# Kernel optimization log

Measured on AMD Instinct MI355X. Metric: run time of the kernel, lower is better.

## Reference

```python
import jax, jax.numpy as jnp
import numpy as np

RES = (160, 160, 160)
SCENE_MIN = -1.0
SCENE_SIZE = 2.0
NEAR, FAR = 0.1, 10.0
NUM_SAMPLES = 128


def eval_sh_deg2(dirs):
    # dirs: [N, 3] -> SH basis [N, 9] (degree 2)
    d = dirs / (jnp.linalg.norm(dirs, axis=-1, keepdims=True) + 1e-8)
    x, y, z = d[..., 0], d[..., 1], d[..., 2]
    return jnp.stack([
        0.28209479177387814 * jnp.ones_like(x),
        -0.48860251190291987 * y,
        0.48860251190291987 * z,
        -0.48860251190291987 * x,
        1.0925484305920792 * x * y,
        -1.0925484305920792 * y * z,
        0.31539156525252005 * (2.0 * z * z - x * x - y * y),
        -1.0925484305920792 * x * z,
        0.5462742152960396 * (x * x - y * y),
    ], axis=-1)


def trilinear_interp(coords, density, sh_coeffs):
    # coords: [N, 3] world coords; grids indexed [z, y, x] as in the torch source
    res = jnp.asarray(RES, dtype=coords.dtype)
    vox = (coords - SCENE_MIN) / SCENE_SIZE * res
    vox = jnp.clip(vox, 0.0, res - 1.0)
    fl = jnp.floor(vox)
    frac = vox - fl
    fl = fl.astype(jnp.int32)
    x0, y0, z0 = fl[..., 0], fl[..., 1], fl[..., 2]
    x1 = jnp.minimum(x0 + 1, RES[0] - 1)
    y1 = jnp.minimum(y0 + 1, RES[1] - 1)
    z1 = jnp.minimum(z0 + 1, RES[2] - 1)
    dx, dy, dz = frac[..., 0], frac[..., 1], frac[..., 2]
    corners = [
        ((z0, y0, x0), (1 - dx) * (1 - dy) * (1 - dz)),
        ((z1, y0, x0), (1 - dx) * (1 - dy) * dz),
        ((z0, y1, x0), (1 - dx) * dy * (1 - dz)),
        ((z1, y1, x0), (1 - dx) * dy * dz),
        ((z0, y0, x1), dx * (1 - dy) * (1 - dz)),
        ((z1, y0, x1), dx * (1 - dy) * dz),
        ((z0, y1, x1), dx * dy * (1 - dz)),
        ((z1, y1, x1), dx * dy * dz),
    ]
    dens = 0.0
    sh = 0.0
    for (zi, yi, xi), w in corners:
        dens = dens + w * density[zi, yi, xi]
        sh = sh + w[:, None, None] * sh_coeffs[zi, yi, xi]
    return dens, sh


def plenoxel_forward(ray_origins, ray_directions, density, sh_coeffs):
    R = ray_origins.shape[0]
    t_vals = jnp.linspace(NEAR, FAR, NUM_SAMPLES, dtype=ray_origins.dtype)  # [S]
    # points: [R, S, 3]
    points = ray_origins[:, None, :] + t_vals[None, :, None] * ray_directions[:, None, :]
    pts = points.reshape(-1, 3)
    dens, sh = trilinear_interp(pts, density, sh_coeffs)  # [N], [N,3,9]
    dirs = jnp.broadcast_to(ray_directions[:, None, :], points.shape).reshape(-1, 3)
    basis = eval_sh_deg2(dirs)  # [N, 9]
    colors = jax.nn.sigmoid(jnp.sum(sh * basis[:, None, :], axis=-1))  # [N, 3]
    dens = dens.reshape(R, NUM_SAMPLES)
    colors = colors.reshape(R, NUM_SAMPLES, 3)
    # volume rendering
    dists = t_vals[1:] - t_vals[:-1]
    dists = jnp.concatenate([dists, jnp.full((1,), 1e10, dtype=t_vals.dtype)], axis=0)
    dists = dists[None, :] * jnp.linalg.norm(ray_directions, axis=-1, keepdims=True)  # [R,S]
    alpha = 1.0 - jnp.exp(-jax.nn.relu(dens) * dists)
    trans = jnp.cumprod(1.0 - alpha + 1e-10, axis=-1)
    trans = jnp.concatenate([jnp.ones_like(trans[..., :1]), trans[..., :-1]], axis=-1)
    weights = alpha * trans
    rgb = jnp.sum(weights[..., None] * colors, axis=-2)  # [R,3]
    depth = jnp.sum(weights * t_vals[None, :], axis=-1)  # [R]
    acc = jnp.sum(weights, axis=-1)  # [R]
    return rgb, depth, acc


def setup_inputs() -> dict:
    key = jax.random.key(0)
    k0, k1, k2, k3 = jax.random.split(key, 4)
    R = 4096
    ray_origins = jax.random.uniform(k0, (R, 3), dtype=jnp.float32, minval=-0.5, maxval=0.5)
    ray_directions = jax.random.normal(k1, (R, 3), dtype=jnp.float32)
    ray_directions = ray_directions / jnp.linalg.norm(ray_directions, axis=-1, keepdims=True)
    density = jax.random.uniform(k2, RES, dtype=jnp.float32, minval=-0.1, maxval=0.1)
    sh_coeffs = jax.random.uniform(k3, (*RES, 3, 9), dtype=jnp.float32, minval=-0.1, maxval=0.1)
    sh_coeffs = sh_coeffs.at[..., 0].set(0.5)
    return {"ray_origins": ray_origins, "ray_directions": ray_directions,
            "density": density, "sh_coeffs": sh_coeffs}


def reference(ray_origins, ray_directions, density, sh_coeffs):
    return plenoxel_forward(ray_origins, ray_directions, density, sh_coeffs)
```

## Files before the change

### kernel.cpp

```cpp
#include <hip/hip_runtime.h>
#include <math.h>

#define RES 160
#define NSAMP 128
#define NEAR_T 0.1f
#define FAR_T 10.0f

__global__ __launch_bounds__(NSAMP) void plenoxel_kernel(
    const float* __restrict__ ray_o,
    const float* __restrict__ ray_d,
    const float* __restrict__ density,
    const float* __restrict__ sh,
    float* __restrict__ out_rgb,
    float* __restrict__ out_depth,
    float* __restrict__ out_acc,
    int R)
{
    const int r = blockIdx.x;
    const int s = threadIdx.x;
    const int lane = s & 63;
    if (r >= R) return;

    const float ox = ray_o[r * 3 + 0], oy = ray_o[r * 3 + 1], oz = ray_o[r * 3 + 2];
    const float dx = ray_d[r * 3 + 0], dy = ray_d[r * 3 + 1], dz = ray_d[r * 3 + 2];

    const float dn  = sqrtf(dx * dx + dy * dy + dz * dz);
    const float inv = 1.0f / (dn + 1e-8f);
    const float nx = dx * inv, ny = dy * inv, nz = dz * inv;
    float basis[9];
    basis[0] = 0.28209479177387814f;
    basis[1] = -0.48860251190291987f * ny;
    basis[2] =  0.48860251190291987f * nz;
    basis[3] = -0.48860251190291987f * nx;
    basis[4] =  1.0925484305920792f * nx * ny;
    basis[5] = -1.0925484305920792f * ny * nz;
    basis[6] =  0.31539156525252005f * (2.0f * nz * nz - nx * nx - ny * ny);
    basis[7] = -1.0925484305920792f * nx * nz;
    basis[8] =  0.5462742152960396f * (nx * nx - ny * ny);

    const float step = (FAR_T - NEAR_T) / (float)(NSAMP - 1);
    const float t = NEAR_T + step * (float)s;
    float dist = (s == NSAMP - 1) ? 1e10f : step;
    dist *= dn;

    const float px = ox + t * dx, py = oy + t * dy, pz = oz + t * dz;
    float vx = (px + 1.0f) * 0.5f * (float)RES;
    float vy = (py + 1.0f) * 0.5f * (float)RES;
    float vz = (pz + 1.0f) * 0.5f * (float)RES;
    vx = fminf(fmaxf(vx, 0.0f), (float)(RES - 1));
    vy = fminf(fmaxf(vy, 0.0f), (float)(RES - 1));
    vz = fminf(fmaxf(vz, 0.0f), (float)(RES - 1));
    const float flx = floorf(vx), fly = floorf(vy), flz = floorf(vz);
    const int x0 = (int)flx, y0 = (int)fly, z0 = (int)flz;
    const int x1 = min(x0 + 1, RES - 1);
    const int y1 = min(y0 + 1, RES - 1);
    const int z1 = min(z0 + 1, RES - 1);
    const float fx = vx - flx, fy = vy - fly, fz = vz - flz;

    const float wx[2] = { 1.0f - fx, fx };
    const float wy[2] = { 1.0f - fy, fy };
    const float wz[2] = { 1.0f - fz, fz };
    const int   xi[2] = { x0, x1 };
    const int   yi[2] = { y0, y1 };
    const int   zi[2] = { z0, z1 };

    float dens = 0.0f;
    float c0 = 0.0f, c1 = 0.0f, c2 = 0.0f;

    #pragma unroll
    for (int k = 0; k < 8; ++k) {
        const int xb = (k >> 2) & 1;
        const int yb = (k >> 1) & 1;
        const int zb =  k       & 1;
        const float w = wx[xb] * wy[yb] * wz[zb];
        const int vidx = (zi[zb] * RES + yi[yb]) * RES + xi[xb];
        dens += w * density[vidx];
        const float* base = sh + (size_t)vidx * 27;
        float c[27];
        __builtin_memcpy(c, base, sizeof(c));
        float d0 = 0.0f, d1 = 0.0f, d2 = 0.0f;
        #pragma unroll
        for (int j = 0; j < 9; ++j) {
            d0 += c[j]      * basis[j];
            d1 += c[9 + j]  * basis[j];
            d2 += c[18 + j] * basis[j];
        }
        c0 += w * d0;
        c1 += w * d1;
        c2 += w * d2;
    }

    const float col0 = 1.0f / (1.0f + __expf(-c0));
    const float col1 = 1.0f / (1.0f + __expf(-c1));
    const float col2 = 1.0f / (1.0f + __expf(-c2));

    const float alpha = 1.0f - __expf(-fmaxf(dens, 0.0f) * dist);
    const float om = 1.0f - alpha + 1e-10f;

    float incl = om;
    #pragma unroll
    for (int off = 1; off < 64; off <<= 1) {
        const float u = __shfl_up(incl, off, 64);
        incl *= (lane >= off) ? u : 1.0f;
    }
    float excl = __shfl_up(incl, 1, 64);
    if (lane == 0) excl = 1.0f;

    __shared__ float w0tot;
    if (s == 63) w0tot = incl;
    __syncthreads();
    const float trans = (s < 64) ? excl : excl * w0tot;
    const float wgt = alpha * trans;

    float v0 = wgt * col0, v1 = wgt * col1, v2 = wgt * col2, v3 = wgt * t, v4 = wgt;
    #pragma unroll
    for (int off = 32; off > 0; off >>= 1) {
        v0 += __shfl_down(v0, off, 64);
        v1 += __shfl_down(v1, off, 64);
        v2 += __shfl_down(v2, off, 64);
        v3 += __shfl_down(v3, off, 64);
        v4 += __shfl_down(v4, off, 64);
    }
    __shared__ float part[2][5];
    if (lane == 0) {
        const int wv = s >> 6;
        part[wv][0] = v0; part[wv][1] = v1; part[wv][2] = v2;
        part[wv][3] = v3; part[wv][4] = v4;
    }
    __syncthreads();
    if (s == 0) {
        out_rgb[r * 3 + 0] = part[0][0] + part[1][0];
        out_rgb[r * 3 + 1] = part[0][1] + part[1][1];
        out_rgb[r * 3 + 2] = part[0][2] + part[1][2];
        out_depth[r]       = part[0][3] + part[1][3];
        out_acc[r]         = part[0][4] + part[1][4];
    }
}

extern "C" void kernel_launch(void* const* d_in, const int* in_sizes, int n_in,
                              void* d_out, int out_size, void* d_ws, size_t ws_size,
                              hipStream_t stream) {
    const float* ray_o   = (const float*)d_in[0];
    const float* ray_d   = (const float*)d_in[1];
    const float* density = (const float*)d_in[2];
    const float* sh      = (const float*)d_in[3];
    const int R = in_sizes[0] / 3;

    float* out_rgb   = (float*)d_out;
    float* out_depth = out_rgb + (size_t)R * 3;
    float* out_acc   = out_depth + R;

    plenoxel_kernel<<<R, NSAMP, 0, stream>>>(ray_o, ray_d, density, sh,
                                             out_rgb, out_depth, out_acc, R);
}
```

Before: 536.5 us.

## Split each sample's SH gather across 8 threads with float4 loads

```diff
diff --git a/kernel.cpp b/kernel.cpp
--- a/kernel.cpp
+++ b/kernel.cpp
@@ -6,7 +6,9 @@
 #define NEAR_T 0.1f
 #define FAR_T 10.0f
 
-__global__ __launch_bounds__(NSAMP) void plenoxel_kernel(
+typedef float float4v __attribute__((ext_vector_type(4)));
+
+__global__ __launch_bounds__(1024) void plenoxel_kernel(
     const float* __restrict__ ray_o,
     const float* __restrict__ ray_d,
     const float* __restrict__ density,
@@ -16,9 +18,10 @@
     float* __restrict__ out_acc,
     int R)
 {
-    const int r = blockIdx.x;
-    const int s = threadIdx.x;
-    const int lane = s & 63;
+    const int r   = blockIdx.x;
+    const int tid = threadIdx.x;
+    const int s   = tid >> 3;
+    const int e   = tid & 7;
     if (r >= R) return;
 
     const float ox = ray_o[r * 3 + 0], oy = ray_o[r * 3 + 1], oz = ray_o[r * 3 + 2];
@@ -27,22 +30,34 @@
     const float dn  = sqrtf(dx * dx + dy * dy + dz * dz);
     const float inv = 1.0f / (dn + 1e-8f);
     const float nx = dx * inv, ny = dy * inv, nz = dz * inv;
-    float basis[9];
-    basis[0] = 0.28209479177387814f;
-    basis[1] = -0.48860251190291987f * ny;
-    basis[2] =  0.48860251190291987f * nz;
-    basis[3] = -0.48860251190291987f * nx;
-    basis[4] =  1.0925484305920792f * nx * ny;
-    basis[5] = -1.0925484305920792f * ny * nz;
-    basis[6] =  0.31539156525252005f * (2.0f * nz * nz - nx * nx - ny * ny);
-    basis[7] = -1.0925484305920792f * nx * nz;
-    basis[8] =  0.5462742152960396f * (nx * nx - ny * ny);
+    const float b0 = 0.28209479177387814f;
+    const float b1 = -0.48860251190291987f * ny;
+    const float b2 =  0.48860251190291987f * nz;
+    const float b3 = -0.48860251190291987f * nx;
+    const float b4 =  1.0925484305920792f * nx * ny;
+    const float b5 = -1.0925484305920792f * ny * nz;
+    const float b6 =  0.31539156525252005f * (2.0f * nz * nz - nx * nx - ny * ny);
+    const float b7 = -1.0925484305920792f * nx * nz;
+    const float b8 =  0.5462742152960396f * (nx * nx - ny * ny);
+
+    float4v bLo = {0.f, 0.f, 0.f, 0.f}, bHi = {0.f, 0.f, 0.f, 0.f};
+    int chLo = 3, chHi = 3;
+    switch (e) {
+        case 0: bLo = (float4v){b0, b1, b2, b3}; chLo = 0; break;
+        case 1: bLo = (float4v){b4, b5, b6, b7}; chLo = 0; break;
+        case 2: bLo = (float4v){b8, 0.f, 0.f, 0.f}; bHi = (float4v){0.f, b0, b1, b2};
+                chLo = 0; chHi = 1; break;
+        case 3: bLo = (float4v){b3, b4, b5, b6}; chLo = 1; break;
+        case 4: bLo = (float4v){b7, b8, 0.f, 0.f}; bHi = (float4v){0.f, 0.f, b0, b1};
+                chLo = 1; chHi = 2; break;
+        case 5: bLo = (float4v){b2, b3, b4, b5}; chLo = 2; break;
+        case 6: bLo = (float4v){0.f, b6, b7, b8}; chLo = 2; break;
+        default: break;
+    }
+    const int offE = (e >= 6) ? 23 : 4 * e;
 
     const float step = (FAR_T - NEAR_T) / (float)(NSAMP - 1);
     const float t = NEAR_T + step * (float)s;
-    float dist = (s == NSAMP - 1) ? 1e10f : step;
-    dist *= dn;
-
     const float px = ox + t * dx, py = oy + t * dy, pz = oz + t * dz;
     float vx = (px + 1.0f) * 0.5f * (float)RES;
     float vy = (py + 1.0f) * 0.5f * (float)RES;
@@ -57,78 +72,99 @@
     const int z1 = min(z0 + 1, RES - 1);
     const float fx = vx - flx, fy = vy - fly, fz = vz - flz;
 
-    const float wx[2] = { 1.0f - fx, fx };
-    const float wy[2] = { 1.0f - fy, fy };
-    const float wz[2] = { 1.0f - fz, fz };
-    const int   xi[2] = { x0, x1 };
-    const int   yi[2] = { y0, y1 };
-    const int   zi[2] = { z0, z1 };
+    const float wx0 = 1.0f - fx, wx1 = fx;
+    const float wy0 = 1.0f - fy, wy1 = fy;
+    const float wz0 = 1.0f - fz, wz1 = fz;
 
-    float dens = 0.0f;
-    float c0 = 0.0f, c1 = 0.0f, c2 = 0.0f;
+    const int zy00 = (z0 * RES + y0) * RES;
+    const int zy01 = (z0 * RES + y1) * RES;
+    const int zy10 = (z1 * RES + y0) * RES;
+    const int zy11 = (z1 * RES + y1) * RES;
+    int   vidx[8];
+    float w8[8];
+    vidx[0] = zy00 + x0; w8[0] = wx0 * wy0 * wz0;
+    vidx[1] = zy10 + x0; w8[1] = wx0 * wy0 * wz1;
+    vidx[2] = zy01 + x0; w8[2] = wx0 * wy1 * wz0;
+    vidx[3] = zy11 + x0; w8[3] = wx0 * wy1 * wz1;
+    vidx[4] = zy00 + x1; w8[4] = wx1 * wy0 * wz0;
+    vidx[5] = zy10 + x1; w8[5] = wx1 * wy0 * wz1;
+    vidx[6] = zy01 + x1; w8[6] = wx1 * wy1 * wz0;
+    vidx[7] = zy11 + x1; w8[7] = wx1 * wy1 * wz1;
 
+    float vD = w8[e] * density[vidx[e]];
+
+    float accLo = 0.0f, accHi = 0.0f;
     #pragma unroll
     for (int k = 0; k < 8; ++k) {
-        const int xb = (k >> 2) & 1;
-        const int yb = (k >> 1) & 1;
-        const int zb =  k       & 1;
-        const float w = wx[xb] * wy[yb] * wz[zb];
-        const int vidx = (zi[zb] * RES + yi[yb]) * RES + xi[xb];
-        dens += w * density[vidx];
-        const float* base = sh + (size_t)vidx * 27;
-        float c[27];
-        __builtin_memcpy(c, base, sizeof(c));
-        float d0 = 0.0f, d1 = 0.0f, d2 = 0.0f;
-        #pragma unroll
-        for (int j = 0; j < 9; ++j) {
-            d0 += c[j]      * basis[j];
-            d1 += c[9 + j]  * basis[j];
-            d2 += c[18 + j] * basis[j];
-        }
-        c0 += w * d0;
-        c1 += w * d1;
-        c2 += w * d2;
+        const float* p = sh + (size_t)vidx[k] * 27 + offE;
+        float4v row = *(const float4v*)p;
+        const float tl = row.x * bLo.x + row.y * bLo.y + row.z * bLo.z + row.w * bLo.w;
+        const float th = row.x * bHi.x + row.y * bHi.y + row.z * bHi.z + row.w * bHi.w;
+        accLo = fmaf(tl, w8[k], accLo);
+        accHi = fmaf(th, w8[k], accHi);
     }
 
-    const float col0 = 1.0f / (1.0f + __expf(-c0));
-    const float col1 = 1.0f / (1.0f + __expf(-c1));
-    const float col2 = 1.0f / (1.0f + __expf(-c2));
+    float v0 = ((chLo == 0) ? accLo : 0.0f) + ((chHi == 0) ? accHi : 0.0f);
+    float v1 = ((chLo == 1) ? accLo : 0.0f) + ((chHi == 1) ? accHi : 0.0f);
+    float v2 = ((chLo == 2) ? accLo : 0.0f) + ((chHi == 2) ? accHi : 0.0f);
+    float v3 = vD;
+    #pragma unroll
+    for (int m = 1; m < 8; m <<= 1) {
+        v0 += __shfl_xor(v0, m, 64);
+        v1 += __shfl_xor(v1, m, 64);
+        v2 += __shfl_xor(v2, m, 64);
+        v3 += __shfl_xor(v3, m, 64);
+    }
 
-    const float alpha = 1.0f - __expf(-fmaxf(dens, 0.0f) * dist);
-    const float om = 1.0f - alpha + 1e-10f;
+    __shared__ float4v sdata[NSAMP];
+    if (e == 0) sdata[s] = (float4v){v0, v1, v2, v3};
+    __syncthreads();
 
-    float incl = om;
-    #pragma unroll
-    for (int off = 1; off < 64; off <<= 1) {
-        const float u = __shfl_up(incl, off, 64);
-        incl *= (lane >= off) ? u : 1.0f;
+    float incl = 1.0f, alpha = 0.0f, col0 = 0.f, col1 = 0.f, col2 = 0.f, ts = 0.f;
+    const int lane = tid & 63;
+    if (tid < NSAMP) {
+        const float4v d = sdata[tid];
+        col0 = 1.0f / (1.0f + __expf(-d.x));
+        col1 = 1.0f / (1.0f + __expf(-d.y));
+        col2 = 1.0f / (1.0f + __expf(-d.z));
+        ts = NEAR_T + step * (float)tid;
+        float dist = ((tid == NSAMP - 1) ? 1e10f : step) * dn;
+        alpha = 1.0f - __expf(-fmaxf(d.w, 0.0f) * dist);
+        const float om = 1.0f - alpha + 1e-10f;
+        incl = om;
+        #pragma unroll
+        for (int off = 1; off < 64; off <<= 1) {
+            const float u = __shfl_up(incl, off, 64);
+            incl *= (lane >= off) ? u : 1.0f;
+        }
     }
-    float excl = __shfl_up(incl, 1, 64);
-    if (lane == 0) excl = 1.0f;
+    __shared__ float w0tot;
+    if (tid == 63) w0tot = incl;
+    __syncthreads();
 
-    __shared__ float w0tot;
-    if (s == 63) w0tot = incl;
-    __syncthreads();
-    const float trans = (s < 64) ? excl : excl * w0tot;
-    const float wgt = alpha * trans;
-
-    float v0 = wgt * col0, v1 = wgt * col1, v2 = wgt * col2, v3 = wgt * t, v4 = wgt;
-    #pragma unroll
-    for (int off = 32; off > 0; off >>= 1) {
-        v0 += __shfl_down(v0, off, 64);
-        v1 += __shfl_down(v1, off, 64);
-        v2 += __shfl_down(v2, off, 64);
-        v3 += __shfl_down(v3, off, 64);
-        v4 += __shfl_down(v4, off, 64);
-    }
     __shared__ float part[2][5];
-    if (lane == 0) {
-        const int wv = s >> 6;
-        part[wv][0] = v0; part[wv][1] = v1; part[wv][2] = v2;
-        part[wv][3] = v3; part[wv][4] = v4;
+    if (tid < NSAMP) {
+        float excl = __shfl_up(incl, 1, 64);
+        if (lane == 0) excl = 1.0f;
+        const float trans = (tid < 64) ? excl : excl * w0tot;
+        const float wgt = alpha * trans;
+        float u0 = wgt * col0, u1 = wgt * col1, u2 = wgt * col2, u3 = wgt * ts, u4 = wgt;
+        #pragma unroll
+        for (int off = 32; off > 0; off >>= 1) {
+            u0 += __shfl_down(u0, off, 64);
+            u1 += __shfl_down(u1, off, 64);
+            u2 += __shfl_down(u2, off, 64);
+            u3 += __shfl_down(u3, off, 64);
+            u4 += __shfl_down(u4, off, 64);
+        }
+        if (lane == 0) {
+            const int wv = tid >> 6;
+            part[wv][0] = u0; part[wv][1] = u1; part[wv][2] = u2;
+            part[wv][3] = u3; part[wv][4] = u4;
+        }
     }
     __syncthreads();
-    if (s == 0) {
+    if (tid == 0) {
         out_rgb[r * 3 + 0] = part[0][0] + part[1][0];
         out_rgb[r * 3 + 1] = part[0][1] + part[1][1];
         out_rgb[r * 3 + 2] = part[0][2] + part[1][2];
@@ -150,6 +186,6 @@
     float* out_depth = out_rgb + (size_t)R * 3;
     float* out_acc   = out_depth + R;
 
-    plenoxel_kernel<<<R, NSAMP, 0, stream>>>(ray_o, ray_d, density, sh,
-                                             out_rgb, out_depth, out_acc, R);
+    plenoxel_kernel<<<R, 1024, 0, stream>>>(ray_o, ray_d, density, sh,
+                                            out_rgb, out_depth, out_acc, R);
 }
```

Result: faster. 523.7 us (-2.4%).
